# Kernel tuning notes

Hardware: AMD Instinct MI355X
Metric: run time of the kernel (lower is better)

## Reference

```python
import jax, jax.numpy as jnp
import numpy as np

N_NODES = 100000
N_EDGES = 1600000
IN_DIM = 128
HID = 128
HEADS = 8
NEG_SLOPE = 0.2  # PyG GATConv default


def _gat_layer(x, src, dst, W, a_src, a_dst, bias, heads, n_nodes):
    """One PyG-style GATConv (concat=True). src/dst already include self-loops."""
    out_ch = W.shape[1] // heads
    h = (x @ W).reshape(n_nodes, heads, out_ch)          # [N, H, C]
    alpha_s = jnp.sum(h * a_src, axis=-1)                # [N, H]
    alpha_d = jnp.sum(h * a_dst, axis=-1)                # [N, H]
    e = jax.nn.leaky_relu(alpha_s[src] + alpha_d[dst], negative_slope=NEG_SLOPE)  # [E, H]
    # segment softmax over destination nodes (stable; self-loops guarantee nonempty segments)
    m = jax.lax.stop_gradient(jax.ops.segment_max(e, dst, num_segments=n_nodes))
    ex = jnp.exp(e - m[dst])
    s = jax.ops.segment_sum(ex, dst, num_segments=n_nodes)
    alpha = ex / s[dst]                                  # [E, H]
    msg = h[src] * alpha[:, :, None]                     # [E, H, C]
    out = jax.ops.segment_sum(msg, dst, num_segments=n_nodes)  # [N, H, C]
    return out.reshape(n_nodes, heads * out_ch) + bias


def setup_inputs() -> dict:
    key = jax.random.key(0)
    ks = jax.random.split(key, 12)
    c1 = HID // HEADS  # per-head channels of layer 1
    g = lambda k, shape, fan_in: jax.random.normal(k, shape, dtype=jnp.float32) * (1.0 / np.sqrt(fan_in))
    return {
        "x": jax.random.normal(ks[0], (N_NODES, IN_DIM), dtype=jnp.float32),
        "edge_index": jax.random.randint(ks[1], (2, N_EDGES), 0, N_NODES, dtype=jnp.int32),
        "W1": g(ks[2], (IN_DIM, HEADS * c1), IN_DIM),
        "a_src1": g(ks[3], (HEADS, c1), c1),
        "a_dst1": g(ks[4], (HEADS, c1), c1),
        "b1": jnp.zeros((HEADS * c1,), dtype=jnp.float32),
        "W2": g(ks[5], (HID, HID), HID),
        "a_src2": g(ks[6], (1, HID), HID),
        "a_dst2": g(ks[7], (1, HID), HID),
        "b2": jnp.zeros((HID,), dtype=jnp.float32),
    }


def reference(x, edge_index, W1, a_src1, a_dst1, b1, W2, a_src2, a_dst2, b2):
    n = x.shape[0]
    loops = jnp.arange(n, dtype=edge_index.dtype)  # add_self_loops=True (PyG default)
    src = jnp.concatenate([edge_index[0], loops])
    dst = jnp.concatenate([edge_index[1], loops])
    h = _gat_layer(x, src, dst, W1, a_src1, a_dst1, b1, HEADS, n)
    h = jax.nn.elu(h)  # inter-layer ELU; dropout p=0.0 is a no-op
    out = _gat_layer(h, src, dst, W2, a_src2, a_dst2, b2, 1, n)
    return out
```

## Files before the change

kernel.cpp:

```cpp
#include <hip/hip_runtime.h>
#include <hip/hip_bf16.h>
#include <math.h>

#define NEG_SLOPE 0.2f

typedef _Float16 half8 __attribute__((ext_vector_type(8)));
typedef _Float16 half4 __attribute__((ext_vector_type(4)));
typedef float f32x4 __attribute__((ext_vector_type(4)));

__device__ __forceinline__ float lrelu(float x){ return x > 0.0f ? x : NEG_SLOPE * x; }

__global__ void hist_kernel(const int* __restrict__ dst, int E,
                            int* __restrict__ deg, int rangeSize){
  const int x   = blockIdx.x & 7;
  const int gb  = blockIdx.x >> 3;
  const int nGB = gridDim.x >> 3;
  const int lo = x * rangeSize, hi = lo + rangeSize;
  const int stride = nGB * blockDim.x;
  for (int i = gb * blockDim.x + threadIdx.x; i < E; i += stride){
    int d = dst[i];
    if (d >= lo && d < hi) atomicAdd(&deg[d], 1);
  }
}

__global__ void scan1_kernel(const int* __restrict__ deg, int N,
                             int* __restrict__ rowptr, int* __restrict__ bsum){
  __shared__ int sdata[256];
  int t = threadIdx.x;
  int base = blockIdx.x * 1024;
  int v[4];
  int run = 0;
#pragma unroll
  for (int j = 0; j < 4; ++j){
    int idx = base + t*4 + j;
    int d = (idx < N) ? deg[idx] : 0;
    run += d;
    v[j] = run;
  }
  sdata[t] = run;
  __syncthreads();
  for (int off = 1; off < 256; off <<= 1){
    int x = (t >= off) ? sdata[t - off] : 0;
    __syncthreads();
    sdata[t] += x;
    __syncthreads();
  }
  int prev = (t > 0) ? sdata[t-1] : 0;
#pragma unroll
  for (int j = 0; j < 4; ++j){
    int idx = base + t*4 + j;
    if (idx < N) rowptr[idx + 1] = v[j] + prev;
  }
  if (t == 255) bsum[blockIdx.x] = sdata[255];
}

__global__ void scan2_kernel(int* __restrict__ bsum, int nb){
  if (threadIdx.x == 0 && blockIdx.x == 0){
    int run = 0;
    for (int i = 0; i < nb; ++i){ int x = bsum[i]; bsum[i] = run; run += x; }
  }
}

__global__ void scan3_kernel(int* __restrict__ rowptr, const int* __restrict__ bsum, int N){
  int i = blockIdx.x * blockDim.x + threadIdx.x;
  if (i == 0) rowptr[0] = 0;
  if (i < N) rowptr[i + 1] += bsum[i >> 10];
}

__global__ void scatter_kernel(const int* __restrict__ src, const int* __restrict__ dst, int E,
                               const int* __restrict__ rowptr, int* __restrict__ fill,
                               int* __restrict__ csr_src, int rangeSize){
  const int x   = blockIdx.x & 7;
  const int gb  = blockIdx.x >> 3;
  const int nGB = gridDim.x >> 3;
  const int lo = x * rangeSize, hi = lo + rangeSize;
  const int stride = nGB * blockDim.x;
  for (int i = gb * blockDim.x + threadIdx.x; i < E; i += stride){
    int d = dst[i];
    if (d >= lo && d < hi){
      int pos = rowptr[d] + atomicAdd(&fill[d], 1);
      csr_src[pos] = src[i];
    }
  }
}

__global__ void prep_w(const float* __restrict__ W, _Float16* __restrict__ Wt){
  int t = threadIdx.x;
  for (int i = 0; i < 64; ++i){
    int e = i*256 + t;
    int k = e >> 7, c = e & 127;
    Wt[c*128 + k] = (_Float16)W[e];
  }
}

template<int H, bool CASTF32>
__launch_bounds__(256, 2)
__global__ void gemm_mfma(const void* __restrict__ Aptr, const _Float16* __restrict__ Wt,
                          _Float16* __restrict__ hout,
                          const float* __restrict__ a_src, const float* __restrict__ a_dst,
                          float* __restrict__ alpha_s, float* __restrict__ alpha_d, int N){
  __shared__ __align__(16) _Float16 Xs[128*128];
  __shared__ __align__(16) _Float16 Ws[128*128];
  __shared__ float apart[2][128][2];
  const int t = threadIdx.x;
  const int lane = t & 63;
  const int w = t >> 6;
  const int wr = w & 1, wc = w >> 1;
  const int rowBase = blockIdx.x * 128;
  const int lrow = lane & 15, lk = lane >> 4;

  if (CASTF32){
    const float* A = (const float*)Aptr;
#pragma unroll
    for (int p = 0; p < 16; ++p){
      int flat = p*256 + t;
      int row = flat >> 5, seg = flat & 31;
      int gr = rowBase + row;
      float4 v = (gr < N) ? *(const float4*)(A + (size_t)gr*128 + seg*4)
                          : make_float4(0.f,0.f,0.f,0.f);
      half4 hv = {(_Float16)v.x, (_Float16)v.y, (_Float16)v.z, (_Float16)v.w};
      int byt = (row*256 + seg*8) ^ ((row & 7) << 4);
      *(half4*)((char*)Xs + byt) = hv;
    }
  } else {
    const _Float16* A = (const _Float16*)Aptr;
#pragma unroll
    for (int p = 0; p < 8; ++p){
      int flat = p*256 + t;
      int row = flat >> 4, seg = flat & 15;
      int gr = rowBase + row;
      int4 v = (gr < N) ? *(const int4*)(A + (size_t)gr*128 + seg*8)
                        : make_int4(0,0,0,0);
      int byt = (row*256 + seg*16) ^ ((row & 7) << 4);
      *(int4*)((char*)Xs + byt) = v;
    }
  }
#pragma unroll
  for (int p = 0; p < 8; ++p){
    int flat = p*256 + t;
    int row = flat >> 4, seg = flat & 15;
    int4 v = *(const int4*)(Wt + row*128 + seg*8);
    int byt = (row*256 + seg*16) ^ ((row & 7) << 4);
    *(int4*)((char*)Ws + byt) = v;
  }
  __syncthreads();

  f32x4 acc[4][4];
#pragma unroll
  for (int mf = 0; mf < 4; ++mf)
#pragma unroll
    for (int nf = 0; nf < 4; ++nf) acc[mf][nf] = (f32x4){0.f,0.f,0.f,0.f};

#pragma unroll
  for (int ks = 0; ks < 4; ++ks){
    const int kbyte = ks*64 + lk*16;
    half8 b[4], a[4];
#pragma unroll
    for (int nf = 0; nf < 4; ++nf){
      int row = wr*64 + nf*16 + lrow;
      b[nf] = *(const half8*)((const char*)Xs + ((row*256 + kbyte) ^ ((row & 7) << 4)));
    }
#pragma unroll
    for (int mf = 0; mf < 4; ++mf){
      int col = wc*64 + mf*16 + lrow;
      a[mf] = *(const half8*)((const char*)Ws + ((col*256 + kbyte) ^ ((col & 7) << 4)));
    }
#pragma unroll
    for (int mf = 0; mf < 4; ++mf)
#pragma unroll
      for (int nf = 0; nf < 4; ++nf)
        acc[mf][nf] = __builtin_amdgcn_mfma_f32_16x16x32_f16(a[mf], b[nf], acc[mf][nf], 0, 0, 0);
  }

#pragma unroll
  for (int nf = 0; nf < 4; ++nf){
    int row = rowBase + wr*64 + nf*16 + lrow;
    if (row < N){
#pragma unroll
      for (int mf = 0; mf < 4; ++mf){
        int col = wc*64 + mf*16 + lk*4;
        f32x4 v = acc[mf][nf];
        half4 hv = {(_Float16)v.x, (_Float16)v.y, (_Float16)v.z, (_Float16)v.w};
        *(half4*)(hout + (size_t)row*128 + col) = hv;
      }
    }
  }

  float4 as4[4], ad4[4];
#pragma unroll
  for (int mf = 0; mf < 4; ++mf){
    int cb = wc*64 + mf*16 + lk*4;
    as4[mf] = *(const float4*)(a_src + cb);
    ad4[mf] = *(const float4*)(a_dst + cb);
  }
  if (H == 8){
#pragma unroll
    for (int nf = 0; nf < 4; ++nf){
      int row = rowBase + wr*64 + nf*16 + lrow;
#pragma unroll
      for (int mf = 0; mf < 4; ++mf){
        f32x4 v = acc[mf][nf];
        float ps = v.x*as4[mf].x + v.y*as4[mf].y + v.z*as4[mf].z + v.w*as4[mf].w;
        float pd = v.x*ad4[mf].x + v.y*ad4[mf].y + v.z*ad4[mf].z + v.w*ad4[mf].w;
        ps += __shfl_xor(ps, 16); ps += __shfl_xor(ps, 32);
        pd += __shfl_xor(pd, 16); pd += __shfl_xor(pd, 32);
        if (lane < 16 && row < N){
          int head = wc*4 + mf;
          alpha_s[(size_t)row*8 + head] = ps;
          alpha_d[(size_t)row*8 + head] = pd;
        }
      }
    }
  } else {
#pragma unroll
    for (int nf = 0; nf < 4; ++nf){
      float ps = 0.f, pd = 0.f;
#pragma unroll
      for (int mf = 0; mf < 4; ++mf){
        f32x4 v = acc[mf][nf];
        ps += v.x*as4[mf].x + v.y*as4[mf].y + v.z*as4[mf].z + v.w*as4[mf].w;
        pd += v.x*ad4[mf].x + v.y*ad4[mf].y + v.z*ad4[mf].z + v.w*ad4[mf].w;
      }
      ps += __shfl_xor(ps, 16); ps += __shfl_xor(ps, 32);
      pd += __shfl_xor(pd, 16); pd += __shfl_xor(pd, 32);
      if (lane < 16){
        int rl = wr*64 + nf*16 + lane;
        apart[0][rl][wc] = ps;
        apart[1][rl][wc] = pd;
      }
    }
    __syncthreads();
    if (wc == 0){
      int rl = wr*64 + lane;
      int row = rowBase + rl;
      if (row < N){
        alpha_s[row] = apart[0][rl][0] + apart[0][rl][1];
        alpha_d[row] = apart[1][rl][0] + apart[1][rl][1];
      }
    }
  }
}

__global__ void ex_kernel(const float* __restrict__ as, const float* __restrict__ ad,
                          const int* __restrict__ rowptr, const int* __restrict__ csr,
                          float* __restrict__ ex1, int N){
  int wid = threadIdx.x >> 6, lane = threadIdx.x & 63;
  int n = blockIdx.x * 4 + wid;
  if (n >= N) return;
  int start = rowptr[n], deg = rowptr[n+1] - start;
  float adn = ad[n];
  for (int i = lane; i < deg; i += 64){
    int s = csr[start + i];
    ex1[start + i] = __expf(lrelu(as[s] + adn));
  }
}

template<int H>
__launch_bounds__(256)
__global__ void agg_kernel(const _Float16* __restrict__ hb, const float* __restrict__ alpha_s,
                           const float* __restrict__ alpha_d, const float* __restrict__ ex1,
                           const int* __restrict__ rowptr, const int* __restrict__ csr_src,
                           const float* __restrict__ bias, void* __restrict__ outv, int N){
  int wid = threadIdx.x >> 6, lane = threadIdx.x & 63;
  int n = blockIdx.x * 4 + wid;
  if (n >= N) return;
  int start = rowptr[n];
  int T = rowptr[n + 1] - start + 1;

  const int g  = lane >> 4;
  const int l  = lane & 15;
  const int ch = l * 8;
  const int hm = (H == 8) ? (l >> 1) : 0;
  float ad_m = 0.f, self_ex = 0.f;
  if (H == 8) ad_m = alpha_d[(size_t)n*8 + hm];
  else        self_ex = __expf(lrelu(alpha_s[n] + alpha_d[n]));

  float acc[8];
#pragma unroll
  for (int i = 0; i < 8; ++i) acc[i] = 0.f;
  float ssum = 0.f;

  for (int j = g; j < T; j += 4){
    int s; float ex;
    if (j == 0){
      s = n;
      ex = (H == 8) ? __expf(lrelu(alpha_s[(size_t)n*8 + hm] + ad_m)) : self_ex;
    } else {
      int p = start + j - 1;
      s = csr_src[p];
      ex = (H == 8) ? __expf(lrelu(alpha_s[(size_t)s*8 + hm] + ad_m)) : ex1[p];
    }
    half8 hv = *(const half8*)(hb + (size_t)s*128 + ch);
#pragma unroll
    for (int i = 0; i < 8; ++i) acc[i] += (float)hv[i] * ex;
    ssum += ex;
  }
#pragma unroll
  for (int off = 16; off < 64; off <<= 1){
    ssum += __shfl_xor(ssum, off);
#pragma unroll
    for (int i = 0; i < 8; ++i) acc[i] += __shfl_xor(acc[i], off);
  }

  if (lane < 16){
    float inv = 1.0f / ssum;
    float4 b0 = *(const float4*)(bias + ch);
    float4 b1 = *(const float4*)(bias + ch + 4);
    float o[8] = {acc[0]*inv + b0.x, acc[1]*inv + b0.y, acc[2]*inv + b0.z, acc[3]*inv + b0.w,
                  acc[4]*inv + b1.x, acc[5]*inv + b1.y, acc[6]*inv + b1.z, acc[7]*inv + b1.w};
    if (H == 8){
      half8 ho;
#pragma unroll
      for (int i = 0; i < 8; ++i){
        float e = (o[i] > 0.f) ? o[i] : expm1f(o[i]);
        ho[i] = (_Float16)e;
      }
      *(half8*)((_Float16*)outv + (size_t)n*128 + ch) = ho;
    } else {
      float* out = (float*)outv;
      *(float4*)(out + (size_t)n*128 + ch)     = make_float4(o[0], o[1], o[2], o[3]);
      *(float4*)(out + (size_t)n*128 + ch + 4) = make_float4(o[4], o[5], o[6], o[7]);
    }
  }
}

extern "C" void kernel_launch(void* const* d_in, const int* in_sizes, int n_in,
                              void* d_out, int out_size, void* d_ws, size_t ws_size,
                              hipStream_t stream){
  const float* x      = (const float*)d_in[0];
  const int*   ei     = (const int*)  d_in[1];
  const float* W1     = (const float*)d_in[2];
  const float* a_src1 = (const float*)d_in[3];
  const float* a_dst1 = (const float*)d_in[4];
  const float* b1     = (const float*)d_in[5];
  const float* W2     = (const float*)d_in[6];
  const float* a_src2 = (const float*)d_in[7];
  const float* a_dst2 = (const float*)d_in[8];
  const float* b2     = (const float*)d_in[9];
  float* out = (float*)d_out;

  const int N = in_sizes[0] / 128;
  const int E = in_sizes[1] / 2;
  const int* src = ei;
  const int* dst = ei + E;

  char* ws = (char*)d_ws;
  size_t off = 0;
  auto alloc = [&](size_t bytes) -> void* {
    void* p = ws + off;
    off += (bytes + 255) & ~(size_t)255;
    return p;
  };
  _Float16* hb   = (_Float16*)alloc((size_t)N * 128 * 2);
  _Float16* act  = (_Float16*)alloc((size_t)N * 128 * 2);
  float* asb     = (float*)alloc((size_t)N * 8 * 4);
  float* adb     = (float*)alloc((size_t)N * 8 * 4);
  float* ex1     = (float*)alloc((size_t)E * 4);
  _Float16* Wt1  = (_Float16*)alloc(16384 * 2);
  _Float16* Wt2  = (_Float16*)alloc(16384 * 2);
  int*   csr     = (int*)  alloc((size_t)E * 4);
  int*   rowptr  = (int*)  alloc((size_t)(N + 1) * 4);
  int*   deg     = (int*)  alloc((size_t)N * 4);
  int*   fill    = (int*)  alloc((size_t)N * 4);
  int*   bsum    = (int*)  alloc(4096);

  hipMemsetAsync(deg, 0, (size_t)((char*)bsum - (char*)deg), stream);

  const int nb = (N + 1023) / 1024;
  const int rangeSize = (N + 7) / 8;
  prep_w        <<<1, 256, 0, stream>>>(W1, Wt1);
  prep_w        <<<1, 256, 0, stream>>>(W2, Wt2);
  hist_kernel   <<<2048, 256, 0, stream>>>(dst, E, deg, rangeSize);
  scan1_kernel  <<<nb, 256, 0, stream>>>(deg, N, rowptr, bsum);
  scan2_kernel  <<<1, 64, 0, stream>>>(bsum, nb);
  scan3_kernel  <<<(N + 255)/256, 256, 0, stream>>>(rowptr, bsum, N);
  scatter_kernel<<<2048, 256, 0, stream>>>(src, dst, E, rowptr, fill, csr, rangeSize);

  const int gBlocks  = (N + 127) / 128;
  const int nBlocks4 = (N + 3) / 4;

  gemm_mfma<8, true><<<gBlocks, 256, 0, stream>>>(x, Wt1, hb, a_src1, a_dst1, asb, adb, N);
  agg_kernel<8><<<nBlocks4, 256, 0, stream>>>(hb, asb, adb, nullptr, rowptr, csr, b1, act, N);

  gemm_mfma<1, false><<<gBlocks, 256, 0, stream>>>(act, Wt2, hb, a_src2, a_dst2, asb, adb, N);
  ex_kernel<<<nBlocks4, 256, 0, stream>>>(asb, adb, rowptr, csr, ex1, N);
  agg_kernel<1><<<nBlocks4, 256, 0, stream>>>(hb, asb, adb, ex1, rowptr, csr, b2, out, N);
}
```

Before: 427.0 us.

## Reorder layer-2 to aggregate before GEMM and fold attention vectors into W2

```diff
diff --git a/kernel.cpp b/kernel.cpp
--- a/kernel.cpp
+++ b/kernel.cpp
@@ -84,19 +84,37 @@
   }
 }
 
-__global__ void prep_w(const float* __restrict__ W, _Float16* __restrict__ Wt){
+__global__ void prep_kernel(const float* __restrict__ W1, const float* __restrict__ W2,
+                            const float* __restrict__ as2, const float* __restrict__ ad2,
+                            _Float16* __restrict__ Wt1, _Float16* __restrict__ Wt2,
+                            float* __restrict__ w2s, float* __restrict__ w2d){
   int t = threadIdx.x;
-  for (int i = 0; i < 64; ++i){
-    int e = i*256 + t;
-    int k = e >> 7, c = e & 127;
-    Wt[c*128 + k] = (_Float16)W[e];
-  }
-}
-
-template<int H, bool CASTF32>
+  if (blockIdx.x < 2){
+    const float* W = blockIdx.x ? W2 : W1;
+    _Float16* Wt = blockIdx.x ? Wt2 : Wt1;
+    for (int i = 0; i < 64; ++i){
+      int e = i*256 + t;
+      int k = e >> 7, c = e & 127;
+      Wt[c*128 + k] = (_Float16)W[e];
+    }
+  } else {
+    if (t < 128){
+      float ps = 0.f, pd = 0.f;
+      for (int c = 0; c < 128; ++c){
+        float w = W2[t*128 + c];
+        ps += w * as2[c];
+        pd += w * ad2[c];
+      }
+      w2s[t] = ps;
+      w2d[t] = pd;
+    }
+  }
+}
+
+template<int ALPHA_H, bool CASTF32, bool OUTF32>
 __launch_bounds__(256, 2)
 __global__ void gemm_mfma(const void* __restrict__ Aptr, const _Float16* __restrict__ Wt,
-                          _Float16* __restrict__ hout,
+                          void* __restrict__ outp, const float* __restrict__ bias,
                           const float* __restrict__ a_src, const float* __restrict__ a_dst,
                           float* __restrict__ alpha_s, float* __restrict__ alpha_d, int N){
   __shared__ __align__(16) _Float16 Xs[128*128];
@@ -172,154 +190,205 @@
         acc[mf][nf] = __builtin_amdgcn_mfma_f32_16x16x32_f16(a[mf], b[nf], acc[mf][nf], 0, 0, 0);
   }
 
-#pragma unroll
-  for (int nf = 0; nf < 4; ++nf){
-    int row = rowBase + wr*64 + nf*16 + lrow;
-    if (row < N){
-#pragma unroll
-      for (int mf = 0; mf < 4; ++mf){
-        int col = wc*64 + mf*16 + lk*4;
-        f32x4 v = acc[mf][nf];
-        half4 hv = {(_Float16)v.x, (_Float16)v.y, (_Float16)v.z, (_Float16)v.w};
-        *(half4*)(hout + (size_t)row*128 + col) = hv;
-      }
-    }
-  }
-
-  float4 as4[4], ad4[4];
-#pragma unroll
-  for (int mf = 0; mf < 4; ++mf){
-    int cb = wc*64 + mf*16 + lk*4;
-    as4[mf] = *(const float4*)(a_src + cb);
-    ad4[mf] = *(const float4*)(a_dst + cb);
-  }
-  if (H == 8){
+  if (OUTF32){
+    float* outf = (float*)outp;
+    float4 b4[4];
+#pragma unroll
+    for (int mf = 0; mf < 4; ++mf)
+      b4[mf] = *(const float4*)(bias + wc*64 + mf*16 + lk*4);
 #pragma unroll
     for (int nf = 0; nf < 4; ++nf){
       int row = rowBase + wr*64 + nf*16 + lrow;
-#pragma unroll
-      for (int mf = 0; mf < 4; ++mf){
-        f32x4 v = acc[mf][nf];
-        float ps = v.x*as4[mf].x + v.y*as4[mf].y + v.z*as4[mf].z + v.w*as4[mf].w;
-        float pd = v.x*ad4[mf].x + v.y*ad4[mf].y + v.z*ad4[mf].z + v.w*ad4[mf].w;
+      if (row < N){
+#pragma unroll
+        for (int mf = 0; mf < 4; ++mf){
+          int col = wc*64 + mf*16 + lk*4;
+          f32x4 v = acc[mf][nf];
+          float4 st = make_float4(v.x + b4[mf].x, v.y + b4[mf].y, v.z + b4[mf].z, v.w + b4[mf].w);
+          *(float4*)(outf + (size_t)row*128 + col) = st;
+        }
+      }
+    }
+  } else {
+    _Float16* hout = (_Float16*)outp;
+#pragma unroll
+    for (int nf = 0; nf < 4; ++nf){
+      int row = rowBase + wr*64 + nf*16 + lrow;
+      if (row < N){
+#pragma unroll
+        for (int mf = 0; mf < 4; ++mf){
+          int col = wc*64 + mf*16 + lk*4;
+          f32x4 v = acc[mf][nf];
+          half4 hv = {(_Float16)v.x, (_Float16)v.y, (_Float16)v.z, (_Float16)v.w};
+          *(half4*)(hout + (size_t)row*128 + col) = hv;
+        }
+      }
+    }
+  }
+
+  if (ALPHA_H > 0){
+    float4 as4[4], ad4[4];
+#pragma unroll
+    for (int mf = 0; mf < 4; ++mf){
+      int cb = wc*64 + mf*16 + lk*4;
+      as4[mf] = *(const float4*)(a_src + cb);
+      ad4[mf] = *(const float4*)(a_dst + cb);
+    }
+    if (ALPHA_H == 8){
+#pragma unroll
+      for (int nf = 0; nf < 4; ++nf){
+        int row = rowBase + wr*64 + nf*16 + lrow;
+#pragma unroll
+        for (int mf = 0; mf < 4; ++mf){
+          f32x4 v = acc[mf][nf];
+          float ps = v.x*as4[mf].x + v.y*as4[mf].y + v.z*as4[mf].z + v.w*as4[mf].w;
+          float pd = v.x*ad4[mf].x + v.y*ad4[mf].y + v.z*ad4[mf].z + v.w*ad4[mf].w;
+          ps += __shfl_xor(ps, 16); ps += __shfl_xor(ps, 32);
+          pd += __shfl_xor(pd, 16); pd += __shfl_xor(pd, 32);
+          if (lane < 16 && row < N){
+            int head = wc*4 + mf;
+            alpha_s[(size_t)row*8 + head] = ps;
+            alpha_d[(size_t)row*8 + head] = pd;
+          }
+        }
+      }
+    } else {
+#pragma unroll
+      for (int nf = 0; nf < 4; ++nf){
+        float ps = 0.f, pd = 0.f;
+#pragma unroll
+        for (int mf = 0; mf < 4; ++mf){
+          f32x4 v = acc[mf][nf];
+          ps += v.x*as4[mf].x + v.y*as4[mf].y + v.z*as4[mf].z + v.w*as4[mf].w;
+          pd += v.x*ad4[mf].x + v.y*ad4[mf].y + v.z*ad4[mf].z + v.w*ad4[mf].w;
+        }
         ps += __shfl_xor(ps, 16); ps += __shfl_xor(ps, 32);
         pd += __shfl_xor(pd, 16); pd += __shfl_xor(pd, 32);
-        if (lane < 16 && row < N){
-          int head = wc*4 + mf;
-          alpha_s[(size_t)row*8 + head] = ps;
-          alpha_d[(size_t)row*8 + head] = pd;
-        }
-      }
-    }
-  } else {
-#pragma unroll
-    for (int nf = 0; nf < 4; ++nf){
-      float ps = 0.f, pd = 0.f;
-#pragma unroll
-      for (int mf = 0; mf < 4; ++mf){
-        f32x4 v = acc[mf][nf];
-        ps += v.x*as4[mf].x + v.y*as4[mf].y + v.z*as4[mf].z + v.w*as4[mf].w;
-        pd += v.x*ad4[mf].x + v.y*ad4[mf].y + v.z*ad4[mf].z + v.w*ad4[mf].w;
-      }
-      ps += __shfl_xor(ps, 16); ps += __shfl_xor(ps, 32);
-      pd += __shfl_xor(pd, 16); pd += __shfl_xor(pd, 32);
-      if (lane < 16){
-        int rl = wr*64 + nf*16 + lane;
-        apart[0][rl][wc] = ps;
-        apart[1][rl][wc] = pd;
-      }
-    }
-    __syncthreads();
-    if (wc == 0){
-      int rl = wr*64 + lane;
-      int row = rowBase + rl;
-      if (row < N){
-        alpha_s[row] = apart[0][rl][0] + apart[0][rl][1];
-        alpha_d[row] = apart[1][rl][0] + apart[1][rl][1];
-      }
-    }
-  }
-}
-
-__global__ void ex_kernel(const float* __restrict__ as, const float* __restrict__ ad,
-                          const int* __restrict__ rowptr, const int* __restrict__ csr,
-                          float* __restrict__ ex1, int N){
-  int wid = threadIdx.x >> 6, lane = threadIdx.x & 63;
-  int n = blockIdx.x * 4 + wid;
-  if (n >= N) return;
-  int start = rowptr[n], deg = rowptr[n+1] - start;
-  float adn = ad[n];
-  for (int i = lane; i < deg; i += 64){
-    int s = csr[start + i];
-    ex1[start + i] = __expf(lrelu(as[s] + adn));
-  }
-}
-
-template<int H>
+        if (lane < 16){
+          int rl = wr*64 + nf*16 + lane;
+          apart[0][rl][wc] = ps;
+          apart[1][rl][wc] = pd;
+        }
+      }
+      __syncthreads();
+      if (wc == 0){
+        int rl = wr*64 + lane;
+        int row = rowBase + rl;
+        if (row < N){
+          alpha_s[row] = apart[0][rl][0] + apart[0][rl][1];
+          alpha_d[row] = apart[1][rl][0] + apart[1][rl][1];
+        }
+      }
+    }
+  }
+}
+
+template<int H, bool LAYER1>
 __launch_bounds__(256)
 __global__ void agg_kernel(const _Float16* __restrict__ hb, const float* __restrict__ alpha_s,
-                           const float* __restrict__ alpha_d, const float* __restrict__ ex1,
+                           const float* __restrict__ alpha_d,
                            const int* __restrict__ rowptr, const int* __restrict__ csr_src,
-                           const float* __restrict__ bias, void* __restrict__ outv, int N){
+                           const float* __restrict__ bias,
+                           const float* __restrict__ w2s, const float* __restrict__ w2d,
+                           _Float16* __restrict__ outh,
+                           float* __restrict__ as2, float* __restrict__ ad2, int N){
   int wid = threadIdx.x >> 6, lane = threadIdx.x & 63;
   int n = blockIdx.x * 4 + wid;
   if (n >= N) return;
   int start = rowptr[n];
-  int T = rowptr[n + 1] - start + 1;
+  int deg = rowptr[n + 1] - start;
 
   const int g  = lane >> 4;
   const int l  = lane & 15;
   const int ch = l * 8;
   const int hm = (H == 8) ? (l >> 1) : 0;
-  float ad_m = 0.f, self_ex = 0.f;
-  if (H == 8) ad_m = alpha_d[(size_t)n*8 + hm];
-  else        self_ex = __expf(lrelu(alpha_s[n] + alpha_d[n]));
+  const float ad_m = alpha_d[(size_t)n*H + hm];
 
   float acc[8];
 #pragma unroll
   for (int i = 0; i < 8; ++i) acc[i] = 0.f;
   float ssum = 0.f;
 
-  for (int j = g; j < T; j += 4){
-    int s; float ex;
-    if (j == 0){
-      s = n;
-      ex = (H == 8) ? __expf(lrelu(alpha_s[(size_t)n*8 + hm] + ad_m)) : self_ex;
-    } else {
-      int p = start + j - 1;
-      s = csr_src[p];
-      ex = (H == 8) ? __expf(lrelu(alpha_s[(size_t)s*8 + hm] + ad_m)) : ex1[p];
-    }
-    half8 hv = *(const half8*)(hb + (size_t)s*128 + ch);
+  if (g == 3){
+    float ex = __expf(lrelu(alpha_s[(size_t)n*H + hm] + ad_m));
+    half8 hv = *(const half8*)(hb + (size_t)n*128 + ch);
 #pragma unroll
     for (int i = 0; i < 8; ++i) acc[i] += (float)hv[i] * ex;
     ssum += ex;
   }
+
+  int i = g;
+  for (; i + 4 < deg; i += 8){
+    int s0 = csr_src[start + i];
+    int s1 = csr_src[start + i + 4];
+    float a0 = alpha_s[(size_t)s0*H + hm];
+    float a1 = alpha_s[(size_t)s1*H + hm];
+    half8 h0 = *(const half8*)(hb + (size_t)s0*128 + ch);
+    half8 h1 = *(const half8*)(hb + (size_t)s1*128 + ch);
+    float e0 = __expf(lrelu(a0 + ad_m));
+    float e1 = __expf(lrelu(a1 + ad_m));
+#pragma unroll
+    for (int k = 0; k < 8; ++k) acc[k] += (float)h0[k] * e0;
+#pragma unroll
+    for (int k = 0; k < 8; ++k) acc[k] += (float)h1[k] * e1;
+    ssum += e0 + e1;
+  }
+  if (i < deg){
+    int s0 = csr_src[start + i];
+    float a0 = alpha_s[(size_t)s0*H + hm];
+    half8 h0 = *(const half8*)(hb + (size_t)s0*128 + ch);
+    float e0 = __expf(lrelu(a0 + ad_m));
+#pragma unroll
+    for (int k = 0; k < 8; ++k) acc[k] += (float)h0[k] * e0;
+    ssum += e0;
+  }
+
 #pragma unroll
   for (int off = 16; off < 64; off <<= 1){
     ssum += __shfl_xor(ssum, off);
 #pragma unroll
-    for (int i = 0; i < 8; ++i) acc[i] += __shfl_xor(acc[i], off);
+    for (int k = 0; k < 8; ++k) acc[k] += __shfl_xor(acc[k], off);
   }
 
   if (lane < 16){
     float inv = 1.0f / ssum;
-    float4 b0 = *(const float4*)(bias + ch);
-    float4 b1 = *(const float4*)(bias + ch + 4);
-    float o[8] = {acc[0]*inv + b0.x, acc[1]*inv + b0.y, acc[2]*inv + b0.z, acc[3]*inv + b0.w,
-                  acc[4]*inv + b1.x, acc[5]*inv + b1.y, acc[6]*inv + b1.z, acc[7]*inv + b1.w};
-    if (H == 8){
-      half8 ho;
-#pragma unroll
-      for (int i = 0; i < 8; ++i){
-        float e = (o[i] > 0.f) ? o[i] : expm1f(o[i]);
-        ho[i] = (_Float16)e;
-      }
-      *(half8*)((_Float16*)outv + (size_t)n*128 + ch) = ho;
+    float o[8];
+    if (LAYER1){
+      float4 b0 = *(const float4*)(bias + ch);
+      float4 b1 = *(const float4*)(bias + ch + 4);
+      float bb[8] = {b0.x,b0.y,b0.z,b0.w,b1.x,b1.y,b1.z,b1.w};
+#pragma unroll
+      for (int k = 0; k < 8; ++k){
+        float v = acc[k]*inv + bb[k];
+        o[k] = (v > 0.f) ? v : expm1f(v);
+      }
     } else {
-      float* out = (float*)outv;
-      *(float4*)(out + (size_t)n*128 + ch)     = make_float4(o[0], o[1], o[2], o[3]);
-      *(float4*)(out + (size_t)n*128 + ch + 4) = make_float4(o[4], o[5], o[6], o[7]);
+#pragma unroll
+      for (int k = 0; k < 8; ++k) o[k] = acc[k]*inv;
+    }
+    half8 ho;
+#pragma unroll
+    for (int k = 0; k < 8; ++k) ho[k] = (_Float16)o[k];
+    *(half8*)(outh + (size_t)n*128 + ch) = ho;
+
+    if (LAYER1){
+      float4 s0 = *(const float4*)(w2s + ch);
+      float4 s1 = *(const float4*)(w2s + ch + 4);
+      float4 d0 = *(const float4*)(w2d + ch);
+      float4 d1 = *(const float4*)(w2d + ch + 4);
+      float ps = o[0]*s0.x + o[1]*s0.y + o[2]*s0.z + o[3]*s0.w
+               + o[4]*s1.x + o[5]*s1.y + o[6]*s1.z + o[7]*s1.w;
+      float pd = o[0]*d0.x + o[1]*d0.y + o[2]*d0.z + o[3]*d0.w
+               + o[4]*d1.x + o[5]*d1.y + o[6]*d1.z + o[7]*d1.w;
+#pragma unroll
+      for (int off = 1; off < 16; off <<= 1){
+        ps += __shfl_xor(ps, off);
+        pd += __shfl_xor(pd, off);
+      }
+      if (l == 0){
+        as2[n] = ps;
+        ad2[n] = pd;
+      }
     }
   }
 }
@@ -355,9 +424,12 @@
   _Float16* act  = (_Float16*)alloc((size_t)N * 128 * 2);
   float* asb     = (float*)alloc((size_t)N * 8 * 4);
   float* adb     = (float*)alloc((size_t)N * 8 * 4);
-  float* ex1     = (float*)alloc((size_t)E * 4);
+  float* as2     = (float*)alloc((size_t)N * 4);
+  float* ad2     = (float*)alloc((size_t)N * 4);
   _Float16* Wt1  = (_Float16*)alloc(16384 * 2);
   _Float16* Wt2  = (_Float16*)alloc(16384 * 2);
+  float* w2s     = (float*)alloc(128 * 4);
+  float* w2d     = (float*)alloc(128 * 4);
   int*   csr     = (int*)  alloc((size_t)E * 4);
   int*   rowptr  = (int*)  alloc((size_t)(N + 1) * 4);
   int*   deg     = (int*)  alloc((size_t)N * 4);
@@ -368,8 +440,7 @@
 
   const int nb = (N + 1023) / 1024;
   const int rangeSize = (N + 7) / 8;
-  prep_w        <<<1, 256, 0, stream>>>(W1, Wt1);
-  prep_w        <<<1, 256, 0, stream>>>(W2, Wt2);
+  prep_kernel   <<<3, 256, 0, stream>>>(W1, W2, a_src2, a_dst2, Wt1, Wt2, w2s, w2d);
   hist_kernel   <<<2048, 256, 0, stream>>>(dst, E, deg, rangeSize);
   scan1_kernel  <<<nb, 256, 0, stream>>>(deg, N, rowptr, bsum);
   scan2_kernel  <<<1, 64, 0, stream>>>(bsum, nb);
@@ -379,10 +450,12 @@
   const int gBlocks  = (N + 127) / 128;
   const int nBlocks4 = (N + 3) / 4;
 
-  gemm_mfma<8, true><<<gBlocks, 256, 0, stream>>>(x, Wt1, hb, a_src1, a_dst1, asb, adb, N);
-  agg_kernel<8><<<nBlocks4, 256, 0, stream>>>(hb, asb, adb, nullptr, rowptr, csr, b1, act, N);
-
-  gemm_mfma<1, false><<<gBlocks, 256, 0, stream>>>(act, Wt2, hb, a_src2, a_dst2, asb, adb, N);
-  ex_kernel<<<nBlocks4, 256, 0, stream>>>(asb, adb, rowptr, csr, ex1, N);
-  agg_kernel<1><<<nBlocks4, 256, 0, stream>>>(hb, asb, adb, ex1, rowptr, csr, b2, out, N);
-}
+  gemm_mfma<8, true, false><<<gBlocks, 256, 0, stream>>>(
+      x, Wt1, hb, nullptr, a_src1, a_dst1, asb, adb, N);
+  agg_kernel<8, true><<<nBlocks4, 256, 0, stream>>>(
+      hb, asb, adb, rowptr, csr, b1, w2s, w2d, act, as2, ad2, N);
+  agg_kernel<1, false><<<nBlocks4, 256, 0, stream>>>(
+      act, as2, ad2, rowptr, csr, nullptr, nullptr, nullptr, hb, nullptr, nullptr, N);
+  gemm_mfma<0, false, true><<<gBlocks, 256, 0, stream>>>(
+      hb, Wt2, out, b2, nullptr, nullptr, nullptr, nullptr, N);
+}
```

Result: faster. 371.4 us (-13.0%).
